# Kernel tuning notes

Measured on AMD Instinct MI355X. Metric: run time of the kernel, lower is better.

The kernel has to match this reference:

```python
import jax, jax.numpy as jnp
import numpy as np

HALF_PI = np.float32(np.pi / 2.0)
EPS = 1e-8

def feature_map(x):
    # [B, L] -> [B, L, 2]: standard quantum-inspired embedding
    return jnp.stack([jnp.cos(HALF_PI * x), jnp.sin(HALF_PI * x)], axis=-1)

def setup_inputs() -> dict:
    key = jax.random.key(0)
    k1, k2, k3, k4 = jax.random.split(key, 4)
    B, L, F, D, C = 32768, 256, 2, 32, 10
    x = jax.random.uniform(k1, (B, L), dtype=jnp.float32)
    core0 = jax.random.normal(k2, (F, 1, D), dtype=jnp.float32) * 0.1
    cores_mid = jax.random.normal(k3, (L - 2, F, D, D), dtype=jnp.float32) * 0.1
    coreN = jax.random.normal(k4, (F, D, C), dtype=jnp.float32) * 0.1
    return {"x": x, "core0": core0, "cores_mid": cores_mid, "coreN": coreN}

def reference(x, core0, cores_mid, coreN):
    feats = feature_map(x)                      # [B, L, F]
    # first site: M = v0 @ A0  -> [B, D]
    M0 = jnp.einsum('bf,fd->bd', feats[:, 0, :], core0[:, 0, :])

    # sequential scan over middle sites with per-step L2 normalization
    vs = jnp.transpose(feats[:, 1:-1, :], (1, 0, 2))  # [L-2, B, F]

    def step(M, inputs):
        v, A = inputs                           # v: [B,F], A: [F,D,D]
        M = jnp.einsum('ba,bf,fac->bc', M, v, A)
        M = M / (jnp.linalg.norm(M, axis=1, keepdims=True) + EPS)
        return M, None

    M, _ = jax.lax.scan(step, M0, (vs, cores_mid))

    # last site and readout
    final = jnp.einsum('bf,fac->bac', feats[:, -1, :], coreN)  # [B, D, C]
    logits = jnp.einsum('ba,bac->bc', M, final)                # [B, C]
    return logits
```

## Files before the change

### kernel.cpp

```cpp
#include <hip/hip_runtime.h>
#include <hip/hip_bf16.h>

#define B_TOTAL   32768
#define L_SITES   256
#define N_MID     254
#define HALF_PI_F 1.57079632679489662f
#define EPS_NORM  1e-8f

#define WS_FRAG 0
#define WS_C0   520192
#define WS_CN   520256
#define WS_X    520896
#define WS_FLAG 8909504

typedef short bf16x8 __attribute__((ext_vector_type(8)));
typedef float f32x4  __attribute__((ext_vector_type(4)));

__device__ __forceinline__ unsigned short f2bf(float f) {
    unsigned u = __builtin_bit_cast(unsigned, f);
    u += 0x7FFFu + ((u >> 16) & 1u);
    return (unsigned short)(u >> 16);
}
__device__ __forceinline__ float bf2f(unsigned short h) {
    unsigned u = ((unsigned)h) << 16;
    return __builtin_bit_cast(float, u);
}
__device__ __forceinline__ bf16x8 asbf(uint4 u) {
    return __builtin_bit_cast(bf16x8, u);
}
__device__ __forceinline__ unsigned pkbf2(float a, float b) {
    float2 p; p.x = a; p.y = b;
    __hip_bfloat162 h2 = __float22bfloat162_rn(p);
    unsigned u;
    __builtin_memcpy(&u, &h2, 4);
    return u;
}
__device__ __forceinline__ void split8(const float* v, bf16x8& hi, bf16x8& lo) {
    uint4 H, L;
    unsigned* hp = (unsigned*)&H;
    unsigned* lp = (unsigned*)&L;
    #pragma unroll
    for (int d = 0; d < 4; ++d) {
        float a = v[2 * d], b = v[2 * d + 1];
        unsigned hb = pkbf2(a, b);
        float h0 = __builtin_bit_cast(float, hb << 16);
        float h1 = __builtin_bit_cast(float, hb & 0xFFFF0000u);
        hp[d] = hb;
        lp[d] = pkbf2(a - h0, b - h1);
    }
    hi = __builtin_bit_cast(bf16x8, H);
    lo = __builtin_bit_cast(bf16x8, L);
}
__device__ __forceinline__ bool detect_bf16(const unsigned* x_raw, int lane) {
    unsigned v = x_raw[lane];
    return __ballot((v & 0xFFFFu) >= 0x4000u) == 0ull;
}

__global__ __launch_bounds__(256)
void aux_all(const void* __restrict__ x_in, const void* __restrict__ c0_in,
             const void* __restrict__ am_in, const void* __restrict__ cn_in,
             float* __restrict__ ws) {
    const int lane = threadIdx.x & 63;
    const bool bf = detect_bf16((const unsigned*)x_in, lane);
    const int b = blockIdx.x;

    if (b < 2048) {
        __shared__ float tile[64][65];
        const int bb = (b & 511) * 64;
        const int ll = (b >> 9) * 64;
        #pragma unroll
        for (int k = 0; k < 16; ++k) {
            int idx = threadIdx.x + k * 256;
            int row = idx >> 6, col = idx & 63;
            size_t gi = (size_t)(bb + row) * L_SITES + ll + col;
            float v = bf ? bf2f(((const unsigned short*)x_in)[gi])
                         : ((const float*)x_in)[gi];
            tile[row][col] = v;
        }
        __syncthreads();
        #pragma unroll
        for (int k = 0; k < 16; ++k) {
            int idx = threadIdx.x + k * 256;
            int row = idx >> 6, col = idx & 63;
            ws[WS_X + (size_t)(ll + row) * B_TOTAL + bb + col] = tile[col][row];
        }
    } else if (b < 2556) {
        int i = (b - 2048) * 256 + threadIdx.x;
        if (i < N_MID * 8 * 64) {
            const int l  = i & 63;
            const int q  = (i >> 6) & 7;
            const int t  = i >> 9;
            const int h  = q >> 2;
            const int kh = (q >> 1) & 1;
            const int p  = q & 1;
            const int n  = h * 16 + (l & 15);
            const int kb = (l >> 4) * 8;
            unsigned dw[4];
            #pragma unroll
            for (int d = 0; d < 4; ++d) {
                unsigned e01[2];
                #pragma unroll
                for (int s = 0; s < 2; ++s) {
                    int a = kb + 2 * d + s;
                    size_t idx = ((size_t)(t * 2 + kh) * 32 + a) * 32 + n;
                    float v = bf ? bf2f(((const unsigned short*)am_in)[idx])
                                 : ((const float*)am_in)[idx];
                    unsigned short hi = f2bf(v);
                    e01[s] = (p == 0) ? hi : f2bf(v - bf2f(hi));
                }
                dw[d] = e01[0] | (e01[1] << 16);
            }
            uint4 o; o.x = dw[0]; o.y = dw[1]; o.z = dw[2]; o.w = dw[3];
            ((uint4*)ws)[(size_t)(t * 8 + q) * 64 + l] = o;
        }
    } else {
        for (int i = threadIdx.x; i < 640; i += 256) {
            if (i < 64)
                ws[WS_C0 + i] = bf ? bf2f(((const unsigned short*)c0_in)[i])
                                   : ((const float*)c0_in)[i];
            ws[WS_CN + i] = bf ? bf2f(((const unsigned short*)cn_in)[i])
                               : ((const float*)cn_in)[i];
        }
        if (threadIdx.x == 0)
            *(unsigned*)(ws + WS_FLAG) = bf ? 1u : 0u;
    }
}

__global__ __launch_bounds__(256)
void mps_mfma(const float* __restrict__ ws, void* __restrict__ out) {
    __shared__ float T[4][528];
    const int lane = threadIdx.x & 63;
    const int w    = threadIdx.x >> 6;
    const int r    = lane & 15;
    const int quad = lane >> 4;
    const int b0   = (blockIdx.x * 4 + w) * 16;
    const float* __restrict__ xT = ws + WS_X;
    const uint4* __restrict__ BF = (const uint4*)ws;
    float* __restrict__ Tw = &T[w][0];
    const int i = b0 + r;

    float mm[8];
    {
        float x0 = xT[i];
        float sn, cs; __sincosf(HALF_PI_F * x0, &sn, &cs);
        const float* c0 = ws + WS_C0;
        #pragma unroll
        for (int j = 0; j < 8; ++j) {
            int a = quad * 8 + j;
            mm[j] = cs * c0[a] + sn * c0[32 + a];
        }
    }

#define DO_STEP(CT, ST, Q0, Q1, Q2, Q3, Q4, Q5, Q6, Q7, DONORM)                    \
    {                                                                              \
        float s0[8], s1[8];                                                        \
        _Pragma("unroll")                                                          \
        for (int j = 0; j < 8; ++j) { s0[j] = (CT) * mm[j]; s1[j] = (ST) * mm[j]; }\
        bf16x8 m0h, m0l, m1h, m1l;                                                 \
        split8(s0, m0h, m0l);                                                      \
        split8(s1, m1h, m1l);                                                      \
        const f32x4 z = {0.f, 0.f, 0.f, 0.f};                                      \
        __builtin_amdgcn_s_setprio(1);                                             \
        f32x4 a00 = __builtin_amdgcn_mfma_f32_16x16x32_bf16(m0h, asbf(Q0), z, 0, 0, 0);   \
        a00 = __builtin_amdgcn_mfma_f32_16x16x32_bf16(m0l, asbf(Q0), a00, 0, 0, 0);\
        a00 = __builtin_amdgcn_mfma_f32_16x16x32_bf16(m0h, asbf(Q1), a00, 0, 0, 0);\
        f32x4 a01 = __builtin_amdgcn_mfma_f32_16x16x32_bf16(m1h, asbf(Q2), z, 0, 0, 0);   \
        a01 = __builtin_amdgcn_mfma_f32_16x16x32_bf16(m1l, asbf(Q2), a01, 0, 0, 0);\
        a01 = __builtin_amdgcn_mfma_f32_16x16x32_bf16(m1h, asbf(Q3), a01, 0, 0, 0);\
        f32x4 a10 = __builtin_amdgcn_mfma_f32_16x16x32_bf16(m0h, asbf(Q4), z, 0, 0, 0);   \
        a10 = __builtin_amdgcn_mfma_f32_16x16x32_bf16(m0l, asbf(Q4), a10, 0, 0, 0);\
        a10 = __builtin_amdgcn_mfma_f32_16x16x32_bf16(m0h, asbf(Q5), a10, 0, 0, 0);\
        f32x4 a11 = __builtin_amdgcn_mfma_f32_16x16x32_bf16(m1h, asbf(Q6), z, 0, 0, 0);   \
        a11 = __builtin_amdgcn_mfma_f32_16x16x32_bf16(m1l, asbf(Q6), a11, 0, 0, 0);\
        a11 = __builtin_amdgcn_mfma_f32_16x16x32_bf16(m1h, asbf(Q7), a11, 0, 0, 0);\
        __builtin_amdgcn_s_setprio(0);                                             \
        f32x4 y0 = a00 + a01;                      \
        f32x4 y1 = a10 + a11;                                     \
        _Pragma("unroll")                                                          \
        for (int reg = 0; reg < 4; ++reg) {                                        \
            Tw[(quad * 4 + reg) * 33 + r]      = y0[reg];                          \
            Tw[(quad * 4 + reg) * 33 + 16 + r] = y1[reg];                          \
        }                                                                          \
        _Pragma("unroll")                                                          \
        for (int j = 0; j < 8; ++j) mm[j] = Tw[r * 33 + quad * 8 + j];             \
        if (DONORM) {                                                              \
            float ss = 0.f;                                                        \
            _Pragma("unroll")                                                      \
            for (int j = 0; j < 8; ++j) ss = fmaf(mm[j], mm[j], ss);               \
            ss += __shfl_xor(ss, 16);                                              \
            ss += __shfl_xor(ss, 32);                                              \
            float kk = 1.0f / (sqrtf(ss) + EPS_NORM);                              \
            _Pragma("unroll")                                                      \
            for (int j = 0; j < 8; ++j) mm[j] *= kk;                               \
        }                                                                          \
    }

    float ct0, st0;
    { float xc = xT[(size_t)B_TOTAL + i]; __sincosf(HALF_PI_F * xc, &st0, &ct0); }
    float x1 = xT[(size_t)2 * B_TOTAL + i];

    const uint4* Ba = BF + lane;
    uint4 fa0 = Ba[0],   fa1 = Ba[64],  fa2 = Ba[128], fa3 = Ba[192];
    uint4 fa4 = Ba[256], fa5 = Ba[320], fa6 = Ba[384], fa7 = Ba[448];

    #pragma unroll 1
    for (int t = 0; t < N_MID; t += 2) {
        const uint4* Bb = BF + (size_t)(t + 1) * 512 + lane;
        uint4 fb0 = Bb[0],   fb1 = Bb[64],  fb2 = Bb[128], fb3 = Bb[192];
        uint4 fb4 = Bb[256], fb5 = Bb[320], fb6 = Bb[384], fb7 = Bb[448];
        float x2 = xT[(size_t)(t + 3) * B_TOTAL + i];
        float ct1, st1; __sincosf(HALF_PI_F * x1, &st1, &ct1);

        DO_STEP(ct0, st0, fa0, fa1, fa2, fa3, fa4, fa5, fa6, fa7, false)

        const uint4* Bc = BF + (size_t)(t + 2) * 512 + lane;
        fa0 = Bc[0];   fa1 = Bc[64];  fa2 = Bc[128]; fa3 = Bc[192];
        fa4 = Bc[256]; fa5 = Bc[320]; fa6 = Bc[384]; fa7 = Bc[448];
        int xr = t + 4; if (xr > 255) xr = 255;
        x1 = xT[(size_t)xr * B_TOTAL + i];
        __sincosf(HALF_PI_F * x2, &st0, &ct0);

        DO_STEP(ct1, st1, fb0, fb1, fb2, fb3, fb4, fb5, fb6, fb7,
                (((t + 1) & 7) == 7) || (t + 1 == N_MID - 1))
    }
#undef DO_STEP

    {
        float xN = xT[(size_t)(L_SITES - 1) * B_TOTAL + i];
        float sN, cN; __sincosf(HALF_PI_F * xN, &sN, &cN);
        const float* kn = ws + WS_CN;
        float acc[10];
        #pragma unroll
        for (int c = 0; c < 10; ++c) acc[c] = 0.f;
        #pragma unroll
        for (int j = 0; j < 8; ++j) {
            int a = quad * 8 + j;
            float Ma = mm[j];
            #pragma unroll
            for (int c = 0; c < 10; ++c) {
                float fin = cN * kn[a * 10 + c] + sN * kn[320 + a * 10 + c];
                acc[c] = fmaf(Ma, fin, acc[c]);
            }
        }
        #pragma unroll
        for (int c = 0; c < 10; ++c) {
            acc[c] += __shfl_xor(acc[c], 16);
            acc[c] += __shfl_xor(acc[c], 32);
        }
        const unsigned bf = *(const unsigned*)(ws + WS_FLAG);
        if (quad == 0) {
            if (bf) {
                __hip_bfloat16* o = (__hip_bfloat16*)out;
                #pragma unroll
                for (int c = 0; c < 10; ++c)
                    o[(size_t)(b0 + r) * 10 + c] = __float2bfloat16(acc[c]);
            } else {
                float* o = (float*)out;
                #pragma unroll
                for (int c = 0; c < 10; ++c)
                    o[(size_t)(b0 + r) * 10 + c] = acc[c];
            }
        }
    }
}

extern "C" void kernel_launch(void* const* d_in, const int* in_sizes, int n_in,
                              void* d_out, int out_size, void* d_ws, size_t ws_size,
                              hipStream_t stream) {
    float* ws = (float*)d_ws;
    aux_all<<<2557, 256, 0, stream>>>(d_in[0], d_in[1], d_in[2], d_in[3], ws);
    mps_mfma<<<512, 256, 0, stream>>>(ws, d_out);
}
```

Measured before the change: 267.0 us.

## Swap MFMA operands and permute core layout to drop LDS transpose

Swaps the A/B operands of the bf16 MFMAs so each step's output accumulator is already laid out as the next step's input fragment. The core matrices are pre-permuted with a fixed index permutation, and the initial vector and readout use the same permutation. This removes the per-step shared-memory store/load round trip and the LDS buffer, and it also merges the four accumulators into two interleaved chains. The price is two longer dependent MFMA chains instead of four short ones. Correctness depends on the permutation matching the MFMA output register layout.

Result: faster. 245.0 us (-8.3%).

```diff
diff --git a/kernel.cpp b/kernel.cpp
--- a/kernel.cpp
+++ b/kernel.cpp
@@ -15,6 +15,10 @@
 
 typedef short bf16x8 __attribute__((ext_vector_type(8)));
 typedef float f32x4  __attribute__((ext_vector_type(4)));
+
+__device__ __host__ __forceinline__ int pi_perm(int quad, int j) {
+    return (j < 4) ? (quad * 4 + j) : (16 + quad * 4 + (j - 4));
+}
 
 __device__ __forceinline__ unsigned short f2bf(float f) {
     unsigned u = __builtin_bit_cast(unsigned, f);
@@ -93,7 +97,7 @@
             const int h  = q >> 2;
             const int kh = (q >> 1) & 1;
             const int p  = q & 1;
-            const int n  = h * 16 + (l & 15);
+            const int m  = h * 16 + (l & 15);
             const int kb = (l >> 4) * 8;
             unsigned dw[4];
             #pragma unroll
@@ -101,8 +105,9 @@
                 unsigned e01[2];
                 #pragma unroll
                 for (int s = 0; s < 2; ++s) {
-                    int a = kb + 2 * d + s;
-                    size_t idx = ((size_t)(t * 2 + kh) * 32 + a) * 32 + n;
+                    int k  = kb + 2 * d + s;
+                    int a  = pi_perm(k >> 3, k & 7);
+                    size_t idx = ((size_t)(t * 2 + kh) * 32 + a) * 32 + m;
                     float v = bf ? bf2f(((const unsigned short*)am_in)[idx])
                                  : ((const float*)am_in)[idx];
                     unsigned short hi = f2bf(v);
@@ -128,7 +133,6 @@
 
 __global__ __launch_bounds__(256)
 void mps_mfma(const float* __restrict__ ws, void* __restrict__ out) {
-    __shared__ float T[4][528];
     const int lane = threadIdx.x & 63;
     const int w    = threadIdx.x >> 6;
     const int r    = lane & 15;
@@ -136,7 +140,6 @@
     const int b0   = (blockIdx.x * 4 + w) * 16;
     const float* __restrict__ xT = ws + WS_X;
     const uint4* __restrict__ BF = (const uint4*)ws;
-    float* __restrict__ Tw = &T[w][0];
     const int i = b0 + r;
 
     float mm[8];
@@ -146,7 +149,7 @@
         const float* c0 = ws + WS_C0;
         #pragma unroll
         for (int j = 0; j < 8; ++j) {
-            int a = quad * 8 + j;
+            int a = pi_perm(quad, j);
             mm[j] = cs * c0[a] + sn * c0[32 + a];
         }
     }
@@ -156,33 +159,26 @@
         float s0[8], s1[8];                                                        \
         _Pragma("unroll")                                                          \
         for (int j = 0; j < 8; ++j) { s0[j] = (CT) * mm[j]; s1[j] = (ST) * mm[j]; }\
-        bf16x8 m0h, m0l, m1h, m1l;                                                 \
-        split8(s0, m0h, m0l);                                                      \
-        split8(s1, m1h, m1l);                                                      \
+        bf16x8 b0h, b0l, b1h, b1l;                                                 \
+        split8(s0, b0h, b0l);                                                      \
+        split8(s1, b1h, b1l);                                                      \
         const f32x4 z = {0.f, 0.f, 0.f, 0.f};                                      \
         __builtin_amdgcn_s_setprio(1);                                             \
-        f32x4 a00 = __builtin_amdgcn_mfma_f32_16x16x32_bf16(m0h, asbf(Q0), z, 0, 0, 0);   \
-        a00 = __builtin_amdgcn_mfma_f32_16x16x32_bf16(m0l, asbf(Q0), a00, 0, 0, 0);\
-        a00 = __builtin_amdgcn_mfma_f32_16x16x32_bf16(m0h, asbf(Q1), a00, 0, 0, 0);\
-        f32x4 a01 = __builtin_amdgcn_mfma_f32_16x16x32_bf16(m1h, asbf(Q2), z, 0, 0, 0);   \
-        a01 = __builtin_amdgcn_mfma_f32_16x16x32_bf16(m1l, asbf(Q2), a01, 0, 0, 0);\
-        a01 = __builtin_amdgcn_mfma_f32_16x16x32_bf16(m1h, asbf(Q3), a01, 0, 0, 0);\
-        f32x4 a10 = __builtin_amdgcn_mfma_f32_16x16x32_bf16(m0h, asbf(Q4), z, 0, 0, 0);   \
-        a10 = __builtin_amdgcn_mfma_f32_16x16x32_bf16(m0l, asbf(Q4), a10, 0, 0, 0);\
-        a10 = __builtin_amdgcn_mfma_f32_16x16x32_bf16(m0h, asbf(Q5), a10, 0, 0, 0);\
-        f32x4 a11 = __builtin_amdgcn_mfma_f32_16x16x32_bf16(m1h, asbf(Q6), z, 0, 0, 0);   \
-        a11 = __builtin_amdgcn_mfma_f32_16x16x32_bf16(m1l, asbf(Q6), a11, 0, 0, 0);\
-        a11 = __builtin_amdgcn_mfma_f32_16x16x32_bf16(m1h, asbf(Q7), a11, 0, 0, 0);\
+        f32x4 a0 = __builtin_amdgcn_mfma_f32_16x16x32_bf16(asbf(Q0), b0h, z, 0, 0, 0);    \
+        f32x4 a1 = __builtin_amdgcn_mfma_f32_16x16x32_bf16(asbf(Q4), b0h, z, 0, 0, 0);    \
+        a0 = __builtin_amdgcn_mfma_f32_16x16x32_bf16(asbf(Q1), b0h, a0, 0, 0, 0);  \
+        a1 = __builtin_amdgcn_mfma_f32_16x16x32_bf16(asbf(Q5), b0h, a1, 0, 0, 0);  \
+        a0 = __builtin_amdgcn_mfma_f32_16x16x32_bf16(asbf(Q0), b0l, a0, 0, 0, 0);  \
+        a1 = __builtin_amdgcn_mfma_f32_16x16x32_bf16(asbf(Q4), b0l, a1, 0, 0, 0);  \
+        a0 = __builtin_amdgcn_mfma_f32_16x16x32_bf16(asbf(Q2), b1h, a0, 0, 0, 0);  \
+        a1 = __builtin_amdgcn_mfma_f32_16x16x32_bf16(asbf(Q6), b1h, a1, 0, 0, 0);  \
+        a0 = __builtin_amdgcn_mfma_f32_16x16x32_bf16(asbf(Q3), b1h, a0, 0, 0, 0);  \
+        a1 = __builtin_amdgcn_mfma_f32_16x16x32_bf16(asbf(Q7), b1h, a1, 0, 0, 0);  \
+        a0 = __builtin_amdgcn_mfma_f32_16x16x32_bf16(asbf(Q2), b1l, a0, 0, 0, 0);  \
+        a1 = __builtin_amdgcn_mfma_f32_16x16x32_bf16(asbf(Q6), b1l, a1, 0, 0, 0);  \
         __builtin_amdgcn_s_setprio(0);                                             \
-        f32x4 y0 = a00 + a01;                      \
-        f32x4 y1 = a10 + a11;                                     \
-        _Pragma("unroll")                                                          \
-        for (int reg = 0; reg < 4; ++reg) {                                        \
-            Tw[(quad * 4 + reg) * 33 + r]      = y0[reg];                          \
-            Tw[(quad * 4 + reg) * 33 + 16 + r] = y1[reg];                          \
-        }                                                                          \
-        _Pragma("unroll")                                                          \
-        for (int j = 0; j < 8; ++j) mm[j] = Tw[r * 33 + quad * 8 + j];             \
+        mm[0] = a0[0]; mm[1] = a0[1]; mm[2] = a0[2]; mm[3] = a0[3];                \
+        mm[4] = a1[0]; mm[5] = a1[1]; mm[6] = a1[2]; mm[7] = a1[3];                \
         if (DONORM) {                                                              \
             float ss = 0.f;                                                        \
             _Pragma("unroll")                                                      \
@@ -234,7 +230,7 @@
         for (int c = 0; c < 10; ++c) acc[c] = 0.f;
         #pragma unroll
         for (int j = 0; j < 8; ++j) {
-            int a = quad * 8 + j;
+            int a = pi_perm(quad, j);
             float Ma = mm[j];
             #pragma unroll
             for (int c = 0; c < 10; ++c) {
```
